# Optimization experiments

Hardware: AMD Instinct MI355X
Metric: run time of the kernel (lower is better)

The kernel has to match this reference:

```python
import jax, jax.numpy as jnp
import numpy as np
from jax import lax

# dims: B batch, C=d_model=256, IMG=128, P=4 patch, H=W=32, L=H*W=1024
# D=d_inner=512 (ssm_ratio 2.0), N=d_state=16, R=dt_rank=16, K=4 scan directions
B, C, IMG, P = 2, 256, 128, 4
H = W = IMG // P
L = H * W
D_INNER, N, R, K = 512, 16, 16, 4


def layernorm(x, g, b, eps=1e-5):
    mu = jnp.mean(x, axis=-1, keepdims=True)
    var = jnp.var(x, axis=-1, keepdims=True)
    return (x - mu) * lax.rsqrt(var + eps) * g + b


def setup_inputs() -> dict:
    key = jax.random.key(0)
    ks = jax.random.split(key, 12)
    f = lambda i, shape, s=0.02: jax.random.normal(ks[i], shape, jnp.float32) * s
    A_init = jnp.tile(jnp.arange(1, N + 1, dtype=jnp.float32)[None, None, :], (K, D_INNER, 1))
    return {
        "x": jax.random.normal(ks[0], (B, C, IMG, IMG), jnp.float32),
        "patch_w": f(1, (C, C, P, P)),
        "patch_b": jnp.zeros((C,), jnp.float32),
        "ln_g": jnp.ones((C,), jnp.float32),
        "ln_b": jnp.zeros((C,), jnp.float32),
        "in_w": f(2, (2 * D_INNER, C)),
        "conv_w": f(3, (D_INNER, 1, 3, 3)),
        "conv_b": jnp.zeros((D_INNER,), jnp.float32),
        "xproj_w": f(4, (K, R + 2 * N, D_INNER)),
        "dt_w": f(5, (K, D_INNER, R)),
        "dt_b": f(6, (K, D_INNER), 0.1),
        "A_log": jnp.log(A_init),
        "Ds": jnp.ones((K, D_INNER), jnp.float32),
        "on_g": jnp.ones((D_INNER,), jnp.float32),
        "on_b": jnp.zeros((D_INNER,), jnp.float32),
        "out_w": f(7, (C, D_INNER)),
        "head_w": f(8, (1, C)),
        "head_b": jnp.zeros((1,), jnp.float32),
    }


def _forward(x, patch_w, patch_b, ln_g, ln_b, in_w, conv_w, conv_b, xproj_w,
             dt_w, dt_b, A_log, Ds, on_g, on_b, out_w, head_w, head_b):
    dn = ("NCHW", "OIHW", "NCHW")
    # GRL is identity in forward. Patch embed conv, stride = patch.
    t = lax.conv_general_dilated(x, patch_w, (P, P), "VALID", dimension_numbers=dn)
    t = t + patch_b[None, :, None, None]
    t = jnp.transpose(t, (0, 2, 3, 1))                      # (B,H,W,C)

    # ---- VSS block: t + SS2D(LN(t)) ----
    u = layernorm(t, ln_g, ln_b)
    xz = jnp.einsum("bhwc,ec->bhwe", u, in_w)               # (B,H,W,2D)
    xc, z = jnp.split(xz, 2, axis=-1)
    xc = jnp.transpose(xc, (0, 3, 1, 2))                    # (B,D,H,W)
    xc = lax.conv_general_dilated(xc, conv_w, (1, 1), "SAME",
                                  dimension_numbers=dn, feature_group_count=D_INNER)
    xc = jax.nn.silu(xc + conv_b[None, :, None, None])

    # cross-scan: row-major, col-major, and their reverses -> (B,K,D,L)
    x_hw = xc.reshape(B, D_INNER, L)
    x_wh = jnp.transpose(xc, (0, 1, 3, 2)).reshape(B, D_INNER, L)
    xs = jnp.stack([x_hw, x_wh], axis=1)
    xs = jnp.concatenate([xs, jnp.flip(xs, axis=-1)], axis=1)  # (B,4,D,L)

    x_dbl = jnp.einsum("bkdl,kcd->bkcl", xs, xproj_w)          # (B,K,R+2N,L)
    dts_r = x_dbl[:, :, :R]
    Bs = x_dbl[:, :, R:R + N]                                  # (B,K,N,L)
    Cs = x_dbl[:, :, R + N:]                                   # (B,K,N,L)
    dts = jnp.einsum("bkrl,kdr->bkdl", dts_r, dt_w) + dt_b[None, :, :, None]
    dts = jax.nn.softplus(dts)                                 # (B,K,D,L)

    A = -jnp.exp(A_log)                                        # (K,D,N)
    dA = jnp.exp(dts[:, :, :, None, :] * A[None, :, :, :, None])      # (B,K,D,N,L)
    dBu = (dts * xs)[:, :, :, None, :] * Bs[:, :, None, :, :]         # (B,K,D,N,L)

    dA_t = jnp.moveaxis(dA, -1, 0)        # (L,B,K,D,N)
    dBu_t = jnp.moveaxis(dBu, -1, 0)
    Cs_t = jnp.moveaxis(Cs, -1, 0)        # (L,B,K,N)

    def step(h, inputs):
        dA_i, dBu_i, C_i = inputs
        h = dA_i * h + dBu_i
        y = jnp.einsum("bkdn,bkn->bkd", h, C_i)
        return h, y

    h0 = jnp.zeros((B, K, D_INNER, N), xs.dtype)
    _, ys = lax.scan(step, h0, (dA_t, dBu_t, Cs_t))           # ys: (L,B,K,D)
    ys = jnp.moveaxis(ys, 0, -1)                               # (B,K,D,L)
    ys = ys + Ds[None, :, :, None] * xs

    # cross-merge (invert the 4 scan orders and sum)
    y_rev = jnp.flip(ys[:, 2:], axis=-1)                        # (B,2,D,L)
    y_hw = ys[:, 0] + y_rev[:, 0]
    y_wh = ys[:, 1] + y_rev[:, 1]
    y_wh = jnp.transpose(y_wh.reshape(B, D_INNER, W, H), (0, 1, 3, 2)).reshape(B, D_INNER, L)
    y = (y_hw + y_wh).reshape(B, D_INNER, H, W)
    y = jnp.transpose(y, (0, 2, 3, 1))                          # (B,H,W,D)

    y = layernorm(y, on_g, on_b) * jax.nn.silu(z)
    ss_out = jnp.einsum("bhwd,cd->bhwc", y, out_w)
    t = t + ss_out

    # global average pool + head
    pooled = jnp.mean(t, axis=(1, 2))                           # (B,C)
    return pooled @ head_w.T + head_b


def reference(x, patch_w, patch_b, ln_g, ln_b, in_w, conv_w, conv_b, xproj_w,
              dt_w, dt_b, A_log, Ds, on_g, on_b, out_w, head_w, head_b):
    return _forward(x, patch_w, patch_b, ln_g, ln_b, in_w, conv_w, conv_b, xproj_w,
                    dt_w, dt_b, A_log, Ds, on_g, on_b, out_w, head_w, head_b)
```

## Files before the change

### kernel.cpp

```cpp
#include <hip/hip_runtime.h>
#include <math.h>


typedef __attribute__((ext_vector_type(4))) float f32x4;
typedef __attribute__((ext_vector_type(8))) short bf16x8;

__device__ __forceinline__ ushort bf16_rn(float f) {
  uint u = __float_as_uint(f);
  return (ushort)((u + 0x7fffu + ((u >> 16) & 1u)) >> 16);
}
__device__ __forceinline__ float bf2f(uint us) { return __uint_as_float(us << 16); }
__device__ __forceinline__ uint packbf(float a, float b) {
  return (uint)bf16_rn(a) | ((uint)bf16_rn(b) << 16);
}

__global__ __launch_bounds__(256) void prep_kernel(const float* __restrict__ x,
    ushort* __restrict__ Ap,
    const float* __restrict__ pw, const float* __restrict__ iw,
    const float* __restrict__ ow, const float* __restrict__ xw,
    ushort* __restrict__ pwh,
    ushort* __restrict__ iwh, ushort* __restrict__ iwl,
    ushort* __restrict__ owh, ushort* __restrict__ owl,
    ushort* __restrict__ xwh, ushort* __restrict__ xwl) {
  int bid = blockIdx.x;
  int tid = threadIdx.x;
  if (bid < 2048) {
    __shared__ __align__(16) ushort tile[32][136];
    int b = bid >> 10, hh = (bid >> 5) & 31, c0 = (bid & 31) * 8;
    int ci = tid >> 5, ph = (tid >> 3) & 3, w4 = tid & 7;
    const float* src = x + (((long)(b * 256 + c0 + ci) * 128 + 4 * hh + ph) * 128 + 16 * w4);
    #pragma unroll
    for (int j = 0; j < 4; ++j) {
      float4 v = *(const float4*)(src + 4 * j);
      uint2 pk;
      pk.x = packbf(v.x, v.y);
      pk.y = packbf(v.z, v.w);
      *(uint2*)&tile[w4 * 4 + j][ci * 16 + ph * 4] = pk;
    }
    __syncthreads();
    int w = tid >> 3;
    long rowbase = ((long)(b * 1024 + hh * 32 + w)) * 4096 + c0 * 16;
    #pragma unroll
    for (int i = 0; i < 2; ++i) {
      int gr = (tid & 7) + 8 * i;
      *(uint4*)&Ap[rowbase + gr * 8] = *(const uint4*)&tile[w][gr * 8];
    }
  } else {
    int i = (bid - 2048) * 256 + tid;
    if (i < 1048576) {
      pwh[i] = bf16_rn(pw[i]);
      return;
    }
    const float* src; ushort* hi; ushort* lo; int off;
    if (i < 1310720)      { src = iw; hi = iwh; lo = iwl; off = i - 1048576; }
    else if (i < 1441792) { src = ow; hi = owh; lo = owl; off = i - 1310720; }
    else if (i < 1540096) { src = xw; hi = xwh; lo = xwl; off = i - 1441792; }
    else return;
    float f = src[off];
    ushort h = bf16_rn(f);
    hi[off] = h;
    lo[off] = bf16_rn(f - __uint_as_float(((uint)h) << 16));
  }
}

__global__ __launch_bounds__(512) void mfma_bf(
    const ushort* __restrict__ A, const ushort* __restrict__ Bhi,
    const ushort* __restrict__ Blo, float* __restrict__ Cout, float* __restrict__ C2,
    int M, int N, int K, int kchunk, int mode, int NBM, int NBZ, int uselo)
{
  __shared__ __align__(16) ushort Ah[128 * 64];
  __shared__ __align__(16) ushort Bh[64 * 64];
  __shared__ __align__(16) ushort Bl[64 * 64];
  int tid = threadIdx.x;
  int bid = blockIdx.x;
  int kz = bid % NBZ;
  int n0 = (bid / (NBZ * NBM)) * 64;
  int m0 = ((bid / NBZ) % NBM) * 128;
  int k0 = kz * kchunk;
  int wid = tid >> 6, lane = tid & 63;
  int wm = wid >> 1, wn = wid & 1;
  int lrow = lane & 15, g = lane >> 4;
  f32x4 acc[2][2] = {};
  int nkt = kchunk >> 6;
  for (int kt = 0; kt < nkt; ++kt) {
    int kb = k0 + (kt << 6);
    {
      int gi = tid & 7;
      #pragma unroll
      for (int i = 0; i < 2; ++i) {
        int row = (tid >> 3) + (i << 6);
        uint4 v = *(const uint4*)&A[(long)(m0 + row) * K + kb + gi * 8];
        *(uint4*)&Ah[row * 64 + ((gi ^ (row & 7)) << 3)] = v;
      }
      int row = tid >> 3;
      long off = (long)(n0 + row) * K + kb + gi * 8;
      int la = row * 64 + ((gi ^ (row & 7)) << 3);
      *(uint4*)&Bh[la] = *(const uint4*)&Bhi[off];
      if (uselo) *(uint4*)&Bl[la] = *(const uint4*)&Blo[off];
    }
    __syncthreads();
    #pragma unroll
    for (int kk = 0; kk < 2; ++kk) {
      bf16x8 af[2], bhf[2];
      #pragma unroll
      for (int mi = 0; mi < 2; ++mi) {
        int row = wm * 32 + mi * 16 + lrow;
        af[mi] = *(const bf16x8*)&Ah[row * 64 + ((((kk << 2) + g) ^ (row & 7)) << 3)];
      }
      #pragma unroll
      for (int ni = 0; ni < 2; ++ni) {
        int row = wn * 32 + ni * 16 + lrow;
        int col = (((kk << 2) + g) ^ (row & 7)) << 3;
        bhf[ni] = *(const bf16x8*)&Bh[row * 64 + col];
      }
      #pragma unroll
      for (int mi = 0; mi < 2; ++mi)
        #pragma unroll
        for (int ni = 0; ni < 2; ++ni)
          acc[mi][ni] = __builtin_amdgcn_mfma_f32_16x16x32_bf16(af[mi], bhf[ni], acc[mi][ni], 0, 0, 0);
      if (uselo) {
        #pragma unroll
        for (int ni = 0; ni < 2; ++ni) {
          int row = wn * 32 + ni * 16 + lrow;
          int col = (((kk << 2) + g) ^ (row & 7)) << 3;
          bf16x8 blf = *(const bf16x8*)&Bl[row * 64 + col];
          #pragma unroll
          for (int mi = 0; mi < 2; ++mi)
            acc[mi][ni] = __builtin_amdgcn_mfma_f32_16x16x32_bf16(af[mi], blf, acc[mi][ni], 0, 0, 0);
        }
      }
    }
    __syncthreads();
  }
  int r4 = lane >> 4;
  if (mode == 2) {
    bool xhalf = (n0 < 512);
    ushort* xcb = (ushort*)Cout;
    #pragma unroll
    for (int mi = 0; mi < 2; ++mi)
      #pragma unroll
      for (int ni = 0; ni < 2; ++ni) {
        int n = n0 + wn * 32 + ni * 16 + lrow;
        int mb = m0 + wm * 32 + mi * 16 + r4 * 4;
        int bb = mb >> 10, l = mb & 1023;
        if (xhalf) {
          uint2 o;
          o.x = packbf(acc[mi][ni][0], acc[mi][ni][1]);
          o.y = packbf(acc[mi][ni][2], acc[mi][ni][3]);
          *(uint2*)&xcb[((long)(bb * 512 + n)) * 1024 + l] = o;
        } else {
          #pragma unroll
          for (int r = 0; r < 4; ++r)
            C2[(long)(mb + r) * 512 + (n - 512)] = acc[mi][ni][r];
        }
      }
  } else {
    long zoff = (long)kz * M * N;
    #pragma unroll
    for (int mi = 0; mi < 2; ++mi)
      #pragma unroll
      for (int ni = 0; ni < 2; ++ni) {
        int n = n0 + wn * 32 + ni * 16 + lrow;
        int mb = m0 + wm * 32 + mi * 16 + r4 * 4;
        #pragma unroll
        for (int r = 0; r < 4; ++r)
          Cout[zoff + (long)(mb + r) * N + n] = acc[mi][ni][r];
      }
  }
}

__global__ __launch_bounds__(256) void mfma_x(
    const ushort* __restrict__ A, const ushort* __restrict__ Bhi,
    const ushort* __restrict__ Blo, float* __restrict__ xdbl)
{
  __shared__ __align__(16) ushort Ah[64 * 64];
  __shared__ __align__(16) ushort Bh[48 * 64];
  __shared__ __align__(16) ushort Bl[48 * 64];
  int tid = threadIdx.x;
  int m0 = blockIdx.x * 64;
  int z = blockIdx.y, k = z & 3;
  const ushort* Az = A + (long)z * 524288;
  const ushort* Bhz = Bhi + (long)k * 24576;
  const ushort* Blz = Blo + (long)k * 24576;
  int lane = tid & 63, wv = tid >> 6;
  int lrow = lane & 15, g = lane >> 4;
  f32x4 acc[3] = {};
  for (int kt = 0; kt < 8; ++kt) {
    int kb = kt << 6;
    #pragma unroll
    for (int i = 0; i < 2; ++i) {
      int idx = i * 256 + tid;
      int row = idx >> 3, gi = idx & 7;
      uint4 v = *(const uint4*)&Az[(long)(m0 + row) * 512 + kb + gi * 8];
      *(uint4*)&Ah[row * 64 + ((gi ^ (row & 7)) << 3)] = v;
      if (idx < 384) {
        long off = (long)row * 512 + kb + gi * 8;
        int la = row * 64 + ((gi ^ (row & 7)) << 3);
        *(uint4*)&Bh[la] = *(const uint4*)&Bhz[off];
        *(uint4*)&Bl[la] = *(const uint4*)&Blz[off];
      }
    }
    __syncthreads();
    #pragma unroll
    for (int kk = 0; kk < 2; ++kk) {
      int arow = wv * 16 + lrow;
      bf16x8 af = *(const bf16x8*)&Ah[arow * 64 + ((((kk << 2) + g) ^ (arow & 7)) << 3)];
      #pragma unroll
      for (int ni = 0; ni < 3; ++ni) {
        int brow = ni * 16 + lrow;
        int col = (((kk << 2) + g) ^ (brow & 7)) << 3;
        bf16x8 bh = *(const bf16x8*)&Bh[brow * 64 + col];
        bf16x8 bl = *(const bf16x8*)&Bl[brow * 64 + col];
        acc[ni] = __builtin_amdgcn_mfma_f32_16x16x32_bf16(af, bh, acc[ni], 0, 0, 0);
        acc[ni] = __builtin_amdgcn_mfma_f32_16x16x32_bf16(af, bl, acc[ni], 0, 0, 0);
      }
    }
    __syncthreads();
  }
  float* Cz = xdbl + (long)z * 49152;
  int r4 = lane >> 4;
  #pragma unroll
  for (int ni = 0; ni < 3; ++ni) {
    int n = ni * 16 + lrow;
    int mb = m0 + wv * 16 + r4 * 4;
    #pragma unroll
    for (int r = 0; r < 4; ++r)
      Cz[(long)(mb + r) * 48 + n] = acc[ni][r];
  }
}

__device__ __forceinline__ float blk_sum(float v, float* sm) {
  #pragma unroll
  for (int o = 32; o > 0; o >>= 1) v += __shfl_down(v, o);
  int wid = threadIdx.x >> 6, lane = threadIdx.x & 63;
  __syncthreads();
  if (lane == 0) sm[wid] = v;
  __syncthreads();
  int nw = blockDim.x >> 6;
  float r = 0.f;
  for (int i = 0; i < nw; ++i) r += sm[i];
  return r;
}

__global__ __launch_bounds__(256) void reduce_ln1(const float* __restrict__ P,
    const float* __restrict__ bias, const float* __restrict__ g,
    const float* __restrict__ b, ushort* __restrict__ u,
    const float* __restrict__ hw, float* __restrict__ tpart) {
  __shared__ float sm[8];
  int m = blockIdx.x, c = threadIdx.x;
  float v = bias[c];
  #pragma unroll
  for (int s = 0; s < 8; ++s) v += P[(long)s * 524288 + m * 256 + c];
  float s1 = blk_sum(v, sm);
  float s2 = blk_sum(v * v, sm);
  float s3 = blk_sum(v * hw[c], sm);
  if (c == 0) tpart[m] = s3;
  float mu = s1 * (1.f / 256.f);
  float var = s2 * (1.f / 256.f) - mu * mu;
  float rs = rsqrtf(var + 1e-5f);
  u[(long)m * 256 + c] = bf16_rn((v - mu) * rs * g[c] + b[c]);
}

__global__ __launch_bounds__(256) void reduce_ss(const float* __restrict__ P,
    const float* __restrict__ hw, float* __restrict__ spart) {
  __shared__ float sm[8];
  int bid = blockIdx.x;
  int i = bid * 1024 + threadIdx.x * 4;
  float4 v = make_float4(0.f, 0.f, 0.f, 0.f);
  #pragma unroll
  for (int s = 0; s < 4; ++s) {
    float4 p = *(const float4*)(P + (long)s * 524288 + i);
    v.x += p.x; v.y += p.y; v.z += p.z; v.w += p.w;
  }
  float4 w = *(const float4*)(hw + (i & 255));
  float s = v.x * w.x + v.y * w.y + v.z * w.z + v.w * w.w;
  float tot = blk_sum(s, sm);
  if (threadIdx.x == 0) spart[bid] = tot;
}

__global__ __launch_bounds__(256) void head_final(const float* __restrict__ tpart,
    const float* __restrict__ spart, const float* __restrict__ hb,
    float* __restrict__ out) {
  __shared__ float sm[8];
  int b = blockIdx.x, tid = threadIdx.x;
  float s = 0.f;
  #pragma unroll
  for (int j = 0; j < 4; ++j) s += tpart[b * 1024 + tid * 4 + j];
  s += spart[b * 256 + tid];
  float tot = blk_sum(s, sm);
  if (tid == 0) out[b] = tot * (1.f / 1024.f) + hb[0];
}

__global__ __launch_bounds__(256) void dwconv_kernel(const ushort* __restrict__ xc,
    const float* __restrict__ cw, const float* __restrict__ cb, ushort* __restrict__ out) {
  __shared__ float plane[32][33];
  int d = blockIdx.x, b = blockIdx.y;
  long base = ((long)b * 512 + d) * 1024;
  int tid = threadIdx.x;
  uint2 v = *(const uint2*)&xc[base + tid * 4];
  int h0 = (tid * 4) >> 5, w0 = (tid * 4) & 31;
  plane[h0][w0 + 0] = bf2f(v.x & 0xffff); plane[h0][w0 + 1] = bf2f(v.x >> 16);
  plane[h0][w0 + 2] = bf2f(v.y & 0xffff); plane[h0][w0 + 3] = bf2f(v.y >> 16);
  float w9[9];
  #pragma unroll
  for (int i = 0; i < 9; ++i) w9[i] = cw[d * 9 + i];
  float bias = cb[d];
  __syncthreads();
  float o4[4];
  #pragma unroll
  for (int j = 0; j < 4; ++j) {
    int p = tid * 4 + j, h = p >> 5, w = p & 31;
    float acc = 0.f;
    #pragma unroll
    for (int dh = -1; dh <= 1; ++dh) {
      int hy = h + dh;
      if (hy < 0 || hy > 31) continue;
      #pragma unroll
      for (int dw = -1; dw <= 1; ++dw) {
        int wx = w + dw;
        if (wx < 0 || wx > 31) continue;
        acc += w9[(dh + 1) * 3 + (dw + 1)] * plane[hy][wx];
      }
    }
    acc += bias;
    o4[j] = acc / (1.f + __expf(-acc));
  }
  uint2 o2;
  o2.x = packbf(o4[0], o4[1]);
  o2.y = packbf(o4[2], o4[3]);
  *(uint2*)&out[base + tid * 4] = o2;
}

__global__ __launch_bounds__(256) void build_xsT(const ushort* __restrict__ xca,
    ushort* __restrict__ xsTb) {
  __shared__ ushort tile[32][34];
  int h = blockIdx.x;
  int d0 = blockIdx.y * 32;
  int z = blockIdx.z;
  int b = z >> 2, k = z & 3;
  int tid = threadIdx.x;
  int a = tid >> 5, q = tid & 31;
  #pragma unroll
  for (int i = 0; i < 4; ++i) {
    int di = a + i * 8;
    tile[di][q] = xca[((long)(b * 512 + d0 + di)) * 1024 + h * 32 + q];
  }
  __syncthreads();
  #pragma unroll
  for (int i = 0; i < 4; ++i) {
    int w = a + i * 8;
    int r;
    if (k == 0) r = h * 32 + w;
    else if (k == 1) r = w * 32 + h;
    else if (k == 2) r = 1023 - (h * 32 + w);
    else r = 1023 - (w * 32 + h);
    xsTb[((long)z * 1024 + r) * 512 + d0 + q] = tile[q][w];
  }
}

template<bool FINAL>
__global__ __launch_bounds__(128) void scan_chunk6(
    const float* __restrict__ xdbl, ushort* xsb,
    const float* __restrict__ dtw, const float* __restrict__ dtb,
    const float* __restrict__ A_log, const float* __restrict__ Ds,
    float* __restrict__ dsum, float* __restrict__ hpb)
{
  __shared__ float sdt[32][64];
  __shared__ float sxv[16][64];
  __shared__ float sy[16][64];
  __shared__ float sBC[32][32];
  float (*sR)[16] = (float(*)[16])sy;
  int tid = threadIdx.x;
  int dl = tid >> 1, ng = tid & 1;
  int d0 = blockIdx.x * 64;
  int d = d0 + dl;
  int c = blockIdx.y;
  int z = blockIdx.z;
  int k = z & 3;
  long baseD = (long)z * 524288;
  int l0 = c * 32;
  const float* xdz = xdbl + (long)z * 49152 + (long)l0 * 48;
  #pragma unroll
  for (int i = 0; i < 2; ++i) {
    int idx = i * 128 + tid;
    int l = idx >> 3, q = idx & 7;
    *(float4*)&sBC[l][q * 4] = *(const float4*)(xdz + l * 48 + 16 + q * 4);
  }
  {
    int l = tid >> 2, q = tid & 3;
    *(float4*)&sR[l][q * 4] = *(const float4*)(xdz + l * 48 + q * 4);
  }
  float a[8], h[8];
  #pragma unroll
  for (int j = 0; j < 8; ++j) {
    a[j] = -__expf(A_log[((long)k * 512 + d) * 16 + ng * 8 + j]);
    h[j] = 0.f;
  }
  float4 wr0 = *(const float4*)(dtw + ((long)k * 512 + d) * 16);
  float4 wr1 = *(const float4*)(dtw + ((long)k * 512 + d) * 16 + 4);
  float4 wr2 = *(const float4*)(dtw + ((long)k * 512 + d) * 16 + 8);
  float4 wr3 = *(const float4*)(dtw + ((long)k * 512 + d) * 16 + 12);
  float dbias = dtb[k * 512 + d];
  int gbase = c * 65536 + z * 8192 + d * 16 + ng * 8;
  float Dv = 0.f;
  if (FINAL) {
    #pragma unroll
    for (int j = 0; j < 8; ++j) h[j] = hpb[gbase + j];
    Dv = Ds[k * 512 + d];
  }
  __syncthreads();
  #pragma unroll
  for (int li = 0; li < 16; ++li) {
    int l = ng * 16 + li;
    const float* rr = &sR[l][0];
    float acc = dbias;
    acc += wr0.x * rr[0];  acc += wr0.y * rr[1];  acc += wr0.z * rr[2];  acc += wr0.w * rr[3];
    acc += wr1.x * rr[4];  acc += wr1.y * rr[5];  acc += wr1.z * rr[6];  acc += wr1.w * rr[7];
    acc += wr2.x * rr[8];  acc += wr2.y * rr[9];  acc += wr2.z * rr[10]; acc += wr2.w * rr[11];
    acc += wr3.x * rr[12]; acc += wr3.y * rr[13]; acc += wr3.z * rr[14]; acc += wr3.w * rr[15];
    sdt[l][dl] = (acc > 20.f) ? acc : __logf(1.f + __expf(acc));
  }
  __syncthreads();
  int xli = tid >> 3;
  int xdj = (tid & 7) * 8;
  uint4 rxv = *(const uint4*)&xsb[baseD + (long)(l0 + xli) * 512 + d0 + xdj];
  float dtsum = 0.f;
  for (int t = 0; t < 2; ++t) {
    {
      float4 f0, f1;
      f0.x = bf2f(rxv.x & 0xffff); f0.y = bf2f(rxv.x >> 16);
      f0.z = bf2f(rxv.y & 0xffff); f0.w = bf2f(rxv.y >> 16);
      f1.x = bf2f(rxv.z & 0xffff); f1.y = bf2f(rxv.z >> 16);
      f1.z = bf2f(rxv.w & 0xffff); f1.w = bf2f(rxv.w >> 16);
      *(float4*)&sxv[xli][xdj] = f0;
      *(float4*)&sxv[xli][xdj + 4] = f1;
    }
    __syncthreads();
    if (t == 0)
      rxv = *(const uint4*)&xsb[baseD + (long)(l0 + 16 + xli) * 512 + d0 + xdj];
    #pragma unroll
    for (int li = 0; li < 16; ++li) {
      int lr = t * 16 + li;
      float dt = sdt[lr][dl];
      float xv = sxv[li][dl];
      float w = dt * xv;
      float4 B0 = *(const float4*)&sBC[lr][ng * 8];
      float4 B1 = *(const float4*)&sBC[lr][ng * 8 + 4];
      if (!FINAL) {
        dtsum += dt;
        h[0] = __expf(dt * a[0]) * h[0] + w * B0.x;
        h[1] = __expf(dt * a[1]) * h[1] + w * B0.y;
        h[2] = __expf(dt * a[2]) * h[2] + w * B0.z;
        h[3] = __expf(dt * a[3]) * h[3] + w * B0.w;
        h[4] = __expf(dt * a[4]) * h[4] + w * B1.x;
        h[5] = __expf(dt * a[5]) * h[5] + w * B1.y;
        h[6] = __expf(dt * a[6]) * h[6] + w * B1.z;
        h[7] = __expf(dt * a[7]) * h[7] + w * B1.w;
      } else {
        float4 C0 = *(const float4*)&sBC[lr][16 + ng * 8];
        float4 C1 = *(const float4*)&sBC[lr][16 + ng * 8 + 4];
        float p;
        h[0] = __expf(dt * a[0]) * h[0] + w * B0.x; p  = h[0] * C0.x;
        h[1] = __expf(dt * a[1]) * h[1] + w * B0.y; p += h[1] * C0.y;
        h[2] = __expf(dt * a[2]) * h[2] + w * B0.z; p += h[2] * C0.z;
        h[3] = __expf(dt * a[3]) * h[3] + w * B0.w; p += h[3] * C0.w;
        h[4] = __expf(dt * a[4]) * h[4] + w * B1.x; p += h[4] * C1.x;
        h[5] = __expf(dt * a[5]) * h[5] + w * B1.y; p += h[5] * C1.y;
        h[6] = __expf(dt * a[6]) * h[6] + w * B1.z; p += h[6] * C1.z;
        h[7] = __expf(dt * a[7]) * h[7] + w * B1.w; p += h[7] * C1.w;
        p += __shfl_xor(p, 1);
        if (ng == 0) sy[li][dl] = p + Dv * xv;
      }
    }
    __syncthreads();
    if (FINAL) {
      float4 f0 = *(float4*)&sy[xli][xdj];
      float4 f1 = *(float4*)&sy[xli][xdj + 4];
      uint4 o;
      o.x = packbf(f0.x, f0.y); o.y = packbf(f0.z, f0.w);
      o.z = packbf(f1.x, f1.y); o.w = packbf(f1.z, f1.w);
      *(uint4*)&xsb[baseD + (long)(l0 + t * 16 + xli) * 512 + d0 + xdj] = o;
    }
  }
  if (!FINAL) {
    *(float4*)(hpb + gbase)     = make_float4(h[0], h[1], h[2], h[3]);
    *(float4*)(hpb + gbase + 4) = make_float4(h[4], h[5], h[6], h[7]);
    if (ng == 0) dsum[c * 4096 + z * 512 + d] = dtsum;
  }
}

__global__ __launch_bounds__(256) void scan_prefix(const float* __restrict__ dsum,
    const float* __restrict__ A_log, float* __restrict__ hpb) {
  int g = blockIdx.x * 256 + threadIdx.x;
  int z = g >> 13, n = g & 15;
  int d = (g >> 4) & 511;
  int k = z & 3;
  float a = -__expf(A_log[((long)k * 512 + d) * 16 + n]);
  float h = 0.f;
  #pragma unroll
  for (int c = 0; c < 32; ++c) {
    float P = __expf(dsum[c * 4096 + z * 512 + d] * a);
    float hp = hpb[c * 65536 + g];
    hpb[c * 65536 + g] = h;
    h = P * h + hp;
  }
}

__global__ __launch_bounds__(256) void combine_ln2gate(const ushort* __restrict__ ys,
    const float* __restrict__ zb, ushort* __restrict__ out,
    const float* __restrict__ g, const float* __restrict__ b) {
  __shared__ float sm[8];
  int m = blockIdx.x, tid = threadIdx.x;
  int bb = m >> 10, l = m & 1023;
  int hh = l >> 5, w = l & 31;
  int lw = w * 32 + hh;
  long b4 = (long)bb * 4;
  uint u0 = *(const uint*)&ys[((b4 + 0) * 1024 + l) * 512 + tid * 2];
  uint u1 = *(const uint*)&ys[((b4 + 2) * 1024 + (1023 - l)) * 512 + tid * 2];
  uint u2 = *(const uint*)&ys[((b4 + 1) * 1024 + lw) * 512 + tid * 2];
  uint u3 = *(const uint*)&ys[((b4 + 3) * 1024 + (1023 - lw)) * 512 + tid * 2];
  float v0 = bf2f(u0 & 0xffff) + bf2f(u1 & 0xffff) + bf2f(u2 & 0xffff) + bf2f(u3 & 0xffff);
  float v1 = bf2f(u0 >> 16) + bf2f(u1 >> 16) + bf2f(u2 >> 16) + bf2f(u3 >> 16);
  float s1 = blk_sum(v0 + v1, sm);
  float s2 = blk_sum(v0 * v0 + v1 * v1, sm);
  float mu = s1 * (1.f / 512.f);
  float var = s2 * (1.f / 512.f) - mu * mu;
  float rs = rsqrtf(var + 1e-5f);
  float2 gg = *(const float2*)(g + tid * 2);
  float2 bbv = *(const float2*)(b + tid * 2);
  float2 zz = *(const float2*)(zb + (long)m * 512 + tid * 2);
  float y0 = ((v0 - mu) * rs * gg.x + bbv.x) * (zz.x / (1.f + __expf(-zz.x)));
  float y1 = ((v1 - mu) * rs * gg.y + bbv.y) * (zz.y / (1.f + __expf(-zz.y)));
  *(uint*)&out[(long)m * 512 + tid * 2] = packbf(y0, y1);
}

extern "C" void kernel_launch(void* const* d_in, const int* in_sizes, int n_in,
                              void* d_out, int out_size, void* d_ws, size_t ws_size,
                              hipStream_t stream) {
  const float* x       = (const float*)d_in[0];
  const float* patch_w = (const float*)d_in[1];
  const float* patch_b = (const float*)d_in[2];
  const float* ln_g    = (const float*)d_in[3];
  const float* ln_b    = (const float*)d_in[4];
  const float* in_w    = (const float*)d_in[5];
  const float* conv_w  = (const float*)d_in[6];
  const float* conv_b  = (const float*)d_in[7];
  const float* xproj_w = (const float*)d_in[8];
  const float* dt_w    = (const float*)d_in[9];
  const float* dt_b    = (const float*)d_in[10];
  const float* A_log   = (const float*)d_in[11];
  const float* Ds      = (const float*)d_in[12];
  const float* on_g    = (const float*)d_in[13];
  const float* on_b    = (const float*)d_in[14];
  const float* out_w   = (const float*)d_in[15];
  const float* head_w  = (const float*)d_in[16];
  const float* head_b  = (const float*)d_in[17];

  float* ws = (float*)d_ws;
  float* t_buf   = ws;
  float* u_buf   = t_buf + 524288;
  float* xz_buf  = u_buf + 524288;
  float* xc_buf  = xz_buf + 2097152;
  float* xca_buf = xc_buf + 1048576;
  float* xsT_buf = xca_buf + 1048576;
  float* xdbl_buf= xsT_buf + 4194304;
  float* spl_buf = xdbl_buf + 393216;
  float* tail    = spl_buf + 4194304;
  float*  tpart  = t_buf;
  float*  spart  = t_buf + 2048;
  ushort* A_p    = (ushort*)xsT_buf;
  ushort* pw_hi  = (ushort*)xz_buf;
  float*  z_buf  = xz_buf;
  float*  P_patch= spl_buf;
  float*  P_out  = spl_buf;
  ushort* u_bf   = (ushort*)u_buf;
  ushort* xc_bf  = (ushort*)xc_buf;
  ushort* xca_bf = (ushort*)xca_buf;
  ushort* y_bf   = (ushort*)xca_buf;
  ushort* iw_hi  = (ushort*)tail;
  ushort* iw_lo  = (ushort*)(tail + 131072);
  ushort* ow_hi  = (ushort*)(tail + 262144);
  ushort* ow_lo  = (ushort*)(tail + 327680);
  ushort* xw_hi  = (ushort*)(tail + 393216);
  ushort* xw_lo  = (ushort*)(tail + 442368);
  ushort* xsT_bf = (ushort*)(tail + 491520);
  float*  dsum_buf = tail + 2588672;
  float*  hp_buf   = tail + 2719744;

  prep_kernel<<<8065, 256, 0, stream>>>(x, A_p, patch_w, in_w, out_w, xproj_w,
      pw_hi, iw_hi, iw_lo, ow_hi, ow_lo, xw_hi, xw_lo);
  mfma_bf<<<512, 512, 0, stream>>>(A_p, pw_hi, nullptr, P_patch, nullptr,
      2048, 256, 4096, 512, 0, 16, 8, 0);
  reduce_ln1<<<2048, 256, 0, stream>>>(P_patch, patch_b, ln_g, ln_b, u_bf,
      head_w, tpart);
  mfma_bf<<<256, 512, 0, stream>>>(u_bf, iw_hi, iw_lo, xc_buf, z_buf,
      2048, 1024, 256, 256, 2, 16, 1, 1);
  dwconv_kernel<<<dim3(512, 2), 256, 0, stream>>>(xc_bf, conv_w, conv_b, xca_bf);
  build_xsT<<<dim3(32, 16, 8), 256, 0, stream>>>(xca_bf, xsT_bf);
  mfma_x<<<dim3(16, 8), 256, 0, stream>>>(xsT_bf, xw_hi, xw_lo, xdbl_buf);
  scan_chunk6<false><<<dim3(8, 32, 8), 128, 0, stream>>>(xdbl_buf, xsT_bf,
      dt_w, dt_b, A_log, Ds, dsum_buf, hp_buf);
  scan_prefix<<<256, 256, 0, stream>>>(dsum_buf, A_log, hp_buf);
  scan_chunk6<true><<<dim3(8, 32, 8), 128, 0, stream>>>(xdbl_buf, xsT_bf,
      dt_w, dt_b, A_log, Ds, nullptr, hp_buf);
  combine_ln2gate<<<2048, 256, 0, stream>>>(xsT_bf, z_buf, y_bf, on_g, on_b);
  mfma_bf<<<256, 512, 0, stream>>>(y_bf, ow_hi, ow_lo, P_out, nullptr,
      2048, 256, 512, 128, 0, 16, 4, 1);
  reduce_ss<<<512, 256, 0, stream>>>(P_out, head_w, spart);
  head_final<<<2, 256, 0, stream>>>(tpart, spart, head_b, (float*)d_out);
}
```

Baseline: 127.8 us.

## Fold out_proj and head into a single effective weight vector

Because the mean pool and linear head come right after out_proj, head_w·out_w is precomputed into a 512-element vector. Each token's gated LN output is then dotted directly with it inside combine_ln2gate. This removes the out_proj GEMM, its split-K partial buffers, the bf16 y writeback and the reduce_ss kernel. Precision changes because the projection now runs in fp32 on unrounded y, and the weight folding costs 512 threads a 256-long serial loop in prep.

```diff
diff --git a/kernel.cpp b/kernel.cpp
--- a/kernel.cpp
+++ b/kernel.cpp
@@ -18,10 +18,11 @@
     ushort* __restrict__ Ap,
     const float* __restrict__ pw, const float* __restrict__ iw,
     const float* __restrict__ ow, const float* __restrict__ xw,
+    const float* __restrict__ hw,
     ushort* __restrict__ pwh,
     ushort* __restrict__ iwh, ushort* __restrict__ iwl,
-    ushort* __restrict__ owh, ushort* __restrict__ owl,
-    ushort* __restrict__ xwh, ushort* __restrict__ xwl) {
+    ushort* __restrict__ xwh, ushort* __restrict__ xwl,
+    float* __restrict__ weff) {
   int bid = blockIdx.x;
   int tid = threadIdx.x;
   if (bid < 2048) {
@@ -51,15 +52,23 @@
       pwh[i] = bf16_rn(pw[i]);
       return;
     }
-    const float* src; ushort* hi; ushort* lo; int off;
-    if (i < 1310720)      { src = iw; hi = iwh; lo = iwl; off = i - 1048576; }
-    else if (i < 1441792) { src = ow; hi = owh; lo = owl; off = i - 1310720; }
-    else if (i < 1540096) { src = xw; hi = xwh; lo = xwl; off = i - 1441792; }
-    else return;
-    float f = src[off];
-    ushort h = bf16_rn(f);
-    hi[off] = h;
-    lo[off] = bf16_rn(f - __uint_as_float(((uint)h) << 16));
+    if (i < 1409024) {
+      const float* src; ushort* hi; ushort* lo; int off;
+      if (i < 1310720) { src = iw; hi = iwh; lo = iwl; off = i - 1048576; }
+      else             { src = xw; hi = xwh; lo = xwl; off = i - 1310720; }
+      float f = src[off];
+      ushort h = bf16_rn(f);
+      hi[off] = h;
+      lo[off] = bf16_rn(f - __uint_as_float(((uint)h) << 16));
+      return;
+    }
+    if (i < 1409536) {
+      int k = i - 1409024;
+      float s = 0.f;
+      #pragma unroll 8
+      for (int c = 0; c < 256; ++c) s += ow[c * 512 + k] * hw[c];
+      weff[k] = s;
+    }
   }
 }
 
@@ -261,23 +270,6 @@
   u[(long)m * 256 + c] = bf16_rn((v - mu) * rs * g[c] + b[c]);
 }
 
-__global__ __launch_bounds__(256) void reduce_ss(const float* __restrict__ P,
-    const float* __restrict__ hw, float* __restrict__ spart) {
-  __shared__ float sm[8];
-  int bid = blockIdx.x;
-  int i = bid * 1024 + threadIdx.x * 4;
-  float4 v = make_float4(0.f, 0.f, 0.f, 0.f);
-  #pragma unroll
-  for (int s = 0; s < 4; ++s) {
-    float4 p = *(const float4*)(P + (long)s * 524288 + i);
-    v.x += p.x; v.y += p.y; v.z += p.z; v.w += p.w;
-  }
-  float4 w = *(const float4*)(hw + (i & 255));
-  float s = v.x * w.x + v.y * w.y + v.z * w.z + v.w * w.w;
-  float tot = blk_sum(s, sm);
-  if (threadIdx.x == 0) spart[bid] = tot;
-}
-
 __global__ __launch_bounds__(256) void head_final(const float* __restrict__ tpart,
     const float* __restrict__ spart, const float* __restrict__ hb,
     float* __restrict__ out) {
@@ -285,8 +277,10 @@
   int b = blockIdx.x, tid = threadIdx.x;
   float s = 0.f;
   #pragma unroll
-  for (int j = 0; j < 4; ++j) s += tpart[b * 1024 + tid * 4 + j];
-  s += spart[b * 256 + tid];
+  for (int j = 0; j < 4; ++j) {
+    int m = b * 1024 + tid * 4 + j;
+    s += tpart[m] + spart[m];
+  }
   float tot = blk_sum(s, sm);
   if (tid == 0) out[b] = tot * (1.f / 1024.f) + hb[0];
 }
@@ -507,8 +501,9 @@
 }
 
 __global__ __launch_bounds__(256) void combine_ln2gate(const ushort* __restrict__ ys,
-    const float* __restrict__ zb, ushort* __restrict__ out,
-    const float* __restrict__ g, const float* __restrict__ b) {
+    const float* __restrict__ zb, const float* __restrict__ g,
+    const float* __restrict__ b, const float* __restrict__ weff,
+    float* __restrict__ spart) {
   __shared__ float sm[8];
   int m = blockIdx.x, tid = threadIdx.x;
   int bb = m >> 10, l = m & 1023;
@@ -531,7 +526,9 @@
   float2 zz = *(const float2*)(zb + (long)m * 512 + tid * 2);
   float y0 = ((v0 - mu) * rs * gg.x + bbv.x) * (zz.x / (1.f + __expf(-zz.x)));
   float y1 = ((v1 - mu) * rs * gg.y + bbv.y) * (zz.y / (1.f + __expf(-zz.y)));
-  *(uint*)&out[(long)m * 512 + tid * 2] = packbf(y0, y1);
+  float2 we = *(const float2*)(weff + tid * 2);
+  float s3 = blk_sum(y0 * we.x + y1 * we.y, sm);
+  if (tid == 0) spart[m] = s3;
 }
 
 extern "C" void kernel_launch(void* const* d_in, const int* in_sizes, int n_in,
@@ -572,23 +569,20 @@
   ushort* pw_hi  = (ushort*)xz_buf;
   float*  z_buf  = xz_buf;
   float*  P_patch= spl_buf;
-  float*  P_out  = spl_buf;
   ushort* u_bf   = (ushort*)u_buf;
   ushort* xc_bf  = (ushort*)xc_buf;
   ushort* xca_bf = (ushort*)xca_buf;
-  ushort* y_bf   = (ushort*)xca_buf;
   ushort* iw_hi  = (ushort*)tail;
   ushort* iw_lo  = (ushort*)(tail + 131072);
-  ushort* ow_hi  = (ushort*)(tail + 262144);
-  ushort* ow_lo  = (ushort*)(tail + 327680);
-  ushort* xw_hi  = (ushort*)(tail + 393216);
-  ushort* xw_lo  = (ushort*)(tail + 442368);
-  ushort* xsT_bf = (ushort*)(tail + 491520);
-  float*  dsum_buf = tail + 2588672;
-  float*  hp_buf   = tail + 2719744;
-
-  prep_kernel<<<8065, 256, 0, stream>>>(x, A_p, patch_w, in_w, out_w, xproj_w,
-      pw_hi, iw_hi, iw_lo, ow_hi, ow_lo, xw_hi, xw_lo);
+  ushort* xw_hi  = (ushort*)(tail + 262144);
+  ushort* xw_lo  = (ushort*)(tail + 311296);
+  float*  weff_buf = tail + 360448;
+  ushort* xsT_bf = (ushort*)(tail + 360960);
+  float*  dsum_buf = tail + 2458112;
+  float*  hp_buf   = tail + 2589184;
+
+  prep_kernel<<<7554, 256, 0, stream>>>(x, A_p, patch_w, in_w, out_w, xproj_w,
+      head_w, pw_hi, iw_hi, iw_lo, xw_hi, xw_lo, weff_buf);
   mfma_bf<<<512, 512, 0, stream>>>(A_p, pw_hi, nullptr, P_patch, nullptr,
       2048, 256, 4096, 512, 0, 16, 8, 0);
   reduce_ln1<<<2048, 256, 0, stream>>>(P_patch, patch_b, ln_g, ln_b, u_bf,
@@ -603,9 +597,7 @@
   scan_prefix<<<256, 256, 0, stream>>>(dsum_buf, A_log, hp_buf);
   scan_chunk6<true><<<dim3(8, 32, 8), 128, 0, stream>>>(xdbl_buf, xsT_bf,
       dt_w, dt_b, A_log, Ds, nullptr, hp_buf);
-  combine_ln2gate<<<2048, 256, 0, stream>>>(xsT_bf, z_buf, y_bf, on_g, on_b);
-  mfma_bf<<<256, 512, 0, stream>>>(y_bf, ow_hi, ow_lo, P_out, nullptr,
-      2048, 256, 512, 128, 0, 16, 4, 1);
-  reduce_ss<<<512, 256, 0, stream>>>(P_out, head_w, spart);
+  combine_ln2gate<<<2048, 256, 0, stream>>>(xsT_bf, z_buf, on_g, on_b,
+      weff_buf, spart);
   head_final<<<2, 256, 0, stream>>>(tpart, spart, head_b, (float*)d_out);
 }
```

New measurement: 132.1 us. 3.4% more time.
